# Performance work log

Measured on AMD Instinct MI355X. Metric: run time of the kernel, lower is better.

## Reference

```python
import jax, jax.numpy as jnp
import numpy as np

H, K, D, M = 16, 64, 1024, 4096
S, B = 2048, 4
EPS = 1e-5


def _ln(x, g, b):
    mu = jnp.mean(x, axis=-1, keepdims=True)
    var = jnp.var(x, axis=-1, keepdims=True)
    return (x - mu) / jnp.sqrt(var + EPS) * g + b


def setup_inputs() -> dict:
    key = jax.random.key(0)
    ks = jax.random.split(key, 8)
    std = 0.02
    x = jax.random.normal(ks[0], (S, B, D), jnp.float32)
    mask = jnp.zeros((S, S), jnp.float32)  # additive attention mask, broadcasts over (H*B, S, S)
    wq = jax.random.normal(ks[1], (H * K, D), jnp.float32) * std
    wk = jax.random.normal(ks[2], (H * K, D), jnp.float32) * std
    wv = jax.random.normal(ks[3], (H * K, D), jnp.float32) * std
    wc = jax.random.normal(ks[4], (D, H * K), jnp.float32) * std
    w1_w = jax.random.normal(ks[5], (M, D), jnp.float32) * std
    w1_b = jnp.zeros((M,), jnp.float32)
    w2_w = jax.random.normal(ks[6], (D, M), jnp.float32) * std
    w2_b = jnp.zeros((D,), jnp.float32)
    ln1_g = jnp.ones((D,), jnp.float32)
    ln1_b = jnp.zeros((D,), jnp.float32)
    ln2_g = jnp.ones((D,), jnp.float32)
    ln2_b = jnp.zeros((D,), jnp.float32)
    return dict(x=x, mask=mask, wq=wq, wk=wk, wv=wv, wc=wc, w1_w=w1_w, w1_b=w1_b,
                w2_w=w2_w, w2_b=w2_b, ln1_g=ln1_g, ln1_b=ln1_b, ln2_g=ln2_g, ln2_b=ln2_b)


def reference(x, mask, wq, wk, wv, wc, w1_w, w1_b, w2_w, w2_b, ln1_g, ln1_b, ln2_g, ln2_b):
    s, b, _ = x.shape
    q = (x @ wq.T).reshape(s, b, H, K)
    k = (x @ wk.T).reshape(s, b, H, K)
    v = (x @ wv.T).reshape(s, b, H, K)
    # scores: (B, H, S, S); mask (S, S) broadcasts over batch and heads as in torch
    scores = jnp.einsum('sbhk,tbhk->bhst', q, k) / jnp.sqrt(jnp.float32(K)) + mask
    alpha = jax.nn.softmax(scores, axis=-1)
    av = jnp.einsum('bhst,tbhk->sbhk', alpha, v).reshape(s, b, H * K)
    u = _ln(av @ wc.T + x, ln1_g, ln1_b)
    z = jax.nn.relu(u @ w1_w.T + w1_b) @ w2_w.T + w2_b
    return _ln(z + u, ln2_g, ln2_b)
```

## Files before the change

### kernel.cpp

```cpp
#include <hip/hip_runtime.h>
#include <math.h>

#define H_  16
#define K_  64
#define D_  1024
#define M_  4096
#define S_  2048
#define B_  4
#define N_  8192
#define HK_ 1024

typedef __attribute__((ext_vector_type(8))) short bfrag;
typedef __attribute__((ext_vector_type(4))) float f4;

typedef __attribute__((address_space(1))) const void g_void;
typedef __attribute__((address_space(3))) void s_void;

__device__ __forceinline__ float bf2f(unsigned short u){
  union { unsigned int i; float f; } x; x.i = ((unsigned int)u) << 16; return x.f;
}
__device__ __forceinline__ unsigned short f2bf(float f){
  unsigned int u = __float_as_uint(f);
  return (unsigned short)((u + 0x7fffu + ((u >> 16) & 1u)) >> 16);
}
__device__ __forceinline__ unsigned int pack2(float a, float b){
  return (unsigned int)f2bf(a) | ((unsigned int)f2bf(b) << 16);
}
__device__ __forceinline__ void gload16(const void* g, void* l){
  __builtin_amdgcn_global_load_lds((g_void*)g, (s_void*)l, 16, 0, 0);
}

__global__ __launch_bounds__(256) void castk(const float* __restrict__ in,
                                             unsigned short* __restrict__ out){
  int i = (blockIdx.x * 256 + threadIdx.x) * 4;
  float4 v = *(const float4*)(in + i);
  *(uint2*)(out + i) = make_uint2(pack2(v.x, v.y), pack2(v.z, v.w));
}

__global__ __launch_bounds__(256) void castw4(
    const float* __restrict__ a, const float* __restrict__ b,
    const float* __restrict__ c, const float* __restrict__ d,
    unsigned short* __restrict__ out){
  const int blk = blockIdx.x;
  const int seg = blk >> 10;
  const float* src = (seg == 0) ? a : (seg == 1) ? b : (seg == 2) ? c : d;
  const int rel = ((blk & 1023) * 256 + threadIdx.x) * 4;
  float4 v = *(const float4*)(src + rel);
  *(uint2*)(out + (size_t)seg * 1048576 + rel) = make_uint2(pack2(v.x, v.y), pack2(v.z, v.w));
}

__global__ __launch_bounds__(256) void mscale(const float* __restrict__ in,
                                              float* __restrict__ out){
  int i = (blockIdx.x * 256 + threadIdx.x) * 4;
  float4 v = *(const float4*)(in + i);
  const float c = 1.44269504f;
  v.x *= c; v.y *= c; v.z *= c; v.w *= c;
  *(float4*)(out + i) = v;
}

template<int EPI>
__global__ __launch_bounds__(256) void mgemm(
    const unsigned short* __restrict__ A, const unsigned short* __restrict__ W,
    const float* __restrict__ bias, const void* __restrict__ res,
    unsigned short* __restrict__ C, int Kdim, int Ncols)
{
  __shared__ unsigned short sA[3][4096];
  __shared__ unsigned short sB[3][4096];
  const int tid  = threadIdx.x;
  const int wave = tid >> 6, ln = tid & 63;
  const int lr   = ln & 15, quad = ln >> 4;

  const int nwg = gridDim.x * gridDim.y;
  const int bid = blockIdx.x + gridDim.x * blockIdx.y;
  const int cpx = nwg >> 3;
  const int swz = (bid & 7) * cpx + (bid >> 3);
  const int bx  = swz % gridDim.x, by = swz / gridDim.x;

  const int m0   = by * 128, n0 = bx * 128;
  const int wr   = (wave >> 1) * 64, wc = (wave & 1) * 64;
  const int segr = ln >> 2, segc = (ln & 3) * 8;
  const int sg   = wave * 2;

  const unsigned short* A0 = A + (size_t)(m0 + sg*16      + segr) * Kdim + segc;
  const unsigned short* A1 = A + (size_t)(m0 + sg*16 + 16 + segr) * Kdim + segc;
  const unsigned short* W0 = W + (size_t)(n0 + sg*16      + segr) * Kdim + segc;
  const unsigned short* W1 = W + (size_t)(n0 + sg*16 + 16 + segr) * Kdim + segc;

  const f4 zero = {0.f, 0.f, 0.f, 0.f};
  f4 acc[4][4];
  #pragma unroll
  for (int i=0;i<4;i++)
    #pragma unroll
    for (int j=0;j<4;j++) acc[i][j] = zero;

  auto stage = [&](int buf, int k0){
    gload16(A0 + k0, &sA[buf][sg*512]);
    gload16(A1 + k0, &sA[buf][sg*512 + 512]);
    gload16(W0 + k0, &sB[buf][sg*512]);
    gload16(W1 + k0, &sB[buf][sg*512 + 512]);
  };

  stage(0, 0);
  if (32 < Kdim) stage(1, 32);
  int cur = 0;

  for (int k0 = 0; k0 < Kdim; k0 += 32){
    if (k0 + 32 < Kdim) asm volatile("s_waitcnt vmcnt(4)" ::: "memory");
    else                asm volatile("s_waitcnt vmcnt(0)" ::: "memory");
    __builtin_amdgcn_s_barrier();
    int nxt = cur + 2; if (nxt >= 3) nxt -= 3;
    if (k0 + 64 < Kdim) stage(nxt, k0 + 64);

    bfrag af[4], bf[4];
    #pragma unroll
    for (int i=0;i<4;i++) af[i] = *(const bfrag*)&sA[cur][(wr + i*16 + lr)*32 + quad*8];
    #pragma unroll
    for (int j=0;j<4;j++) bf[j] = *(const bfrag*)&sB[cur][(wc + j*16 + lr)*32 + quad*8];
    #pragma unroll
    for (int i=0;i<4;i++)
      #pragma unroll
      for (int j=0;j<4;j++)
        acc[i][j] = __builtin_amdgcn_mfma_f32_16x16x32_bf16(af[i], bf[j], acc[i][j], 0, 0, 0);
    cur = (cur + 1 == 3) ? 0 : cur + 1;
  }

  #pragma unroll
  for (int i=0;i<4;i++){
    #pragma unroll
    for (int j=0;j<4;j++){
      #pragma unroll
      for (int r=0;r<4;r++){
        const int m = m0 + wr + i*16 + quad*4 + r;
        const int n = n0 + wc + j*16 + lr;
        float t = acc[i][j][r];
        if (EPI == 0){
          const int proj = n >> 10;
          const int s = m >> 2, b = m & 3, h = (n >> 6) & 15, kk = n & 63;
          C[(size_t)proj*8388608 + (((size_t)(b*16 + h)) * S_ + s) * 64 + kk] = f2bf(t);
        } else {
          const size_t off = (size_t)m * Ncols + n;
          if (EPI == 1) t += ((const float*)res)[off];
          if (EPI == 2) t = fmaxf(t + bias[n], 0.f);
          if (EPI == 3) t += bias[n] + bf2f(((const unsigned short*)res)[off]);
          C[off] = f2bf(t);
        }
      }
    }
  }
}

__global__ __launch_bounds__(256) void vtrans(const unsigned short* __restrict__ v,
                                              unsigned short* __restrict__ vT){
  const int tid = threadIdx.x;
  const int wave = tid >> 6, ln = tid & 63;
  const int bh = blockIdx.y;
  const int s  = blockIdx.x * 64 + ln;
  const int d0 = wave * 16;
  unsigned short tmp[16];
  const unsigned short* src = v + ((size_t)bh * S_ + s) * 64 + d0;
  *(uint4*)&tmp[0] = ((const uint4*)src)[0];
  *(uint4*)&tmp[8] = ((const uint4*)src)[1];
  unsigned short* dst = vT + (size_t)bh * 64 * S_ + s;
  #pragma unroll
  for (int e = 0; e < 16; e++)
    dst[(size_t)(d0 + e) * S_] = tmp[e];
}

__global__ __launch_bounds__(256) void fattn(
    const unsigned short* __restrict__ qg, const unsigned short* __restrict__ kg,
    const unsigned short* __restrict__ vT, const float* __restrict__ mb,
    unsigned short* __restrict__ av)
{
  __shared__ unsigned short Ks[2][4096];
  __shared__ unsigned short VTs[2][4096];
  __shared__ unsigned short Ps[4*32*72];
  const int tid  = threadIdx.x;
  const int wave = tid >> 6, ln = tid & 63;
  const int lr   = ln & 15, quad = ln >> 4;
  const int bh   = blockIdx.y;
  const int b    = bh >> 4, h = bh & 15;
  const int s0   = blockIdx.x * 128;
  const size_t base  = (size_t)bh * S_ * 64;
  const size_t tbase = (size_t)bh * 64 * S_;
  const int qw = s0 + wave*32;

  bfrag aq[2][2];
  #pragma unroll
  for (int qb=0;qb<2;qb++)
    #pragma unroll
    for (int hh=0;hh<2;hh++)
      aq[qb][hh] = *(const bfrag*)(qg + base + (size_t)(qw + qb*16 + lr)*64 + hh*32 + quad*8);

  const f4 zero = {0.f, 0.f, 0.f, 0.f};
  f4 acc[2][4];
  #pragma unroll
  for (int qb=0;qb<2;qb++)
    #pragma unroll
    for (int nb=0;nb<4;nb++) acc[qb][nb] = zero;
  float lsum[2][4];
  #pragma unroll
  for (int qb=0;qb<2;qb++)
    #pragma unroll
    for (int r=0;r<4;r++) lsum[qb][r] = 0.f;

  const int strow = wave*16 + (ln >> 3);
  const int scz   = ((ln & 7) ^ (ln >> 3)) * 8;
  const int rxor  = lr & 7;

  unsigned short* const psw = &Ps[wave*2304];

  const float* mrow[2][4];
  #pragma unroll
  for (int qb=0;qb<2;qb++)
    #pragma unroll
    for (int r=0;r<4;r++)
      mrow[qb][r] = mb + (size_t)(qw + qb*16 + quad*4 + r) * S_ + lr;

  auto stage = [&](int bufn, int t0n){
    unsigned short* kd = &Ks[bufn][(wave*16)*64];
    unsigned short* vd = &VTs[bufn][(wave*16)*64];
    gload16(kg + base  + (size_t)(t0n + strow    )*64 + scz, kd);
    gload16(kg + base  + (size_t)(t0n + strow + 8)*64 + scz, kd + 512);
    gload16(vT + tbase + (size_t)(strow    )*S_ + t0n + scz, vd);
    gload16(vT + tbase + (size_t)(strow + 8)*S_ + t0n + scz, vd + 512);
  };

  stage(0, 0);
  int cur = 0;

  for (int t0 = 0; t0 < S_; t0 += 64){
    __syncthreads();

    float mreg[2][4][4];
    #pragma unroll
    for (int qb=0;qb<2;qb++)
      #pragma unroll
      for (int r=0;r<4;r++)
        #pragma unroll
        for (int tb=0;tb<4;tb++)
          mreg[qb][r][tb] = mrow[qb][r][t0 + tb*16];

    if (t0 + 64 < S_) stage(cur ^ 1, t0 + 64);

    const unsigned short* Kc = Ks[cur];
    const unsigned short* Vc = VTs[cur];

    bfrag kf[4][2];
    #pragma unroll
    for (int tb=0;tb<4;tb++)
      #pragma unroll
      for (int hh=0;hh<2;hh++)
        kf[tb][hh] = *(const bfrag*)&Kc[(tb*16 + lr)*64 + (((hh*4 + quad) ^ rxor))*8];

    bfrag vf[4][2];
    #pragma unroll
    for (int nb=0;nb<4;nb++)
      #pragma unroll
      for (int hh=0;hh<2;hh++)
        vf[nb][hh] = *(const bfrag*)&Vc[(nb*16 + lr)*64 + (((hh*4 + quad) ^ rxor))*8];

    #pragma unroll
    for (int qb=0;qb<2;qb++){
      f4 sc[4];
      __builtin_amdgcn_s_setprio(1);
      #pragma unroll
      for (int tb=0;tb<4;tb++){
        f4 t = zero;
        t = __builtin_amdgcn_mfma_f32_16x16x32_bf16(aq[qb][0], kf[tb][0], t, 0, 0, 0);
        t = __builtin_amdgcn_mfma_f32_16x16x32_bf16(aq[qb][1], kf[tb][1], t, 0, 0, 0);
        sc[tb] = t;
      }
      __builtin_amdgcn_s_setprio(0);
      #pragma unroll
      for (int tb=0;tb<4;tb++){
        float p0 = __builtin_amdgcn_exp2f(fmaf(sc[tb][0], 0.18033688f, mreg[qb][0][tb]));
        float p1 = __builtin_amdgcn_exp2f(fmaf(sc[tb][1], 0.18033688f, mreg[qb][1][tb]));
        float p2 = __builtin_amdgcn_exp2f(fmaf(sc[tb][2], 0.18033688f, mreg[qb][2][tb]));
        float p3 = __builtin_amdgcn_exp2f(fmaf(sc[tb][3], 0.18033688f, mreg[qb][3][tb]));
        lsum[qb][0] += p0; lsum[qb][1] += p1;
        lsum[qb][2] += p2; lsum[qb][3] += p3;
        unsigned int pkA, pkB;
        asm("v_cvt_pk_bf16_f32 %0, %1, %2" : "=v"(pkA) : "v"(p0), "v"(p1));
        asm("v_cvt_pk_bf16_f32 %0, %1, %2" : "=v"(pkB) : "v"(p2), "v"(p3));
        unsigned short* pp = &psw[(qb*16 + quad*4)*72 + tb*16 + lr];
        pp[0]   = (unsigned short)pkA;
        pp[72]  = (unsigned short)(pkA >> 16);
        pp[144] = (unsigned short)pkB;
        pp[216] = (unsigned short)(pkB >> 16);
      }
    }

    __builtin_amdgcn_s_setprio(1);
    #pragma unroll
    for (int qb=0;qb<2;qb++){
      bfrag ap0 = *(const bfrag*)&psw[(qb*16 + lr)*72 + quad*8];
      bfrag ap1 = *(const bfrag*)&psw[(qb*16 + lr)*72 + 32 + quad*8];
      #pragma unroll
      for (int nb=0;nb<4;nb++){
        acc[qb][nb] = __builtin_amdgcn_mfma_f32_16x16x32_bf16(ap0, vf[nb][0], acc[qb][nb], 0, 0, 0);
        acc[qb][nb] = __builtin_amdgcn_mfma_f32_16x16x32_bf16(ap1, vf[nb][1], acc[qb][nb], 0, 0, 0);
      }
    }
    __builtin_amdgcn_s_setprio(0);
    cur ^= 1;
  }

  #pragma unroll
  for (int qb=0;qb<2;qb++)
    #pragma unroll
    for (int r=0;r<4;r++){
      float l = lsum[qb][r];
      l += __shfl_xor(l, 1);
      l += __shfl_xor(l, 2);
      l += __shfl_xor(l, 4);
      l += __shfl_xor(l, 8);
      const float inv = 1.f / l;
      const int qrow = qw + qb*16 + quad*4 + r;
      #pragma unroll
      for (int nb=0;nb<4;nb++)
        av[((size_t)qrow * B_ + b) * HK_ + h*64 + nb*16 + lr] = f2bf(acc[qb][nb][r] * inv);
    }
}

template<int OUTF32>
__global__ __launch_bounds__(256) void lnk(
    const unsigned short* __restrict__ pre, const float* __restrict__ g,
    const float* __restrict__ be, void* __restrict__ out)
{
  __shared__ float red[256];
  const int row = blockIdx.x;
  const int tid = threadIdx.x;
  const unsigned short* p = pre + (size_t)row * D_;
  uint2 raw = *(const uint2*)(p + tid*4);
  float x[4] = { bf2f(raw.x & 0xffffu), bf2f(raw.x >> 16),
                 bf2f(raw.y & 0xffffu), bf2f(raw.y >> 16) };
  red[tid] = x[0] + x[1] + x[2] + x[3];
  __syncthreads();
  for (int q = 128; q > 0; q >>= 1){
    if (tid < q) red[tid] += red[tid + q];
    __syncthreads();
  }
  const float mu = red[0] * (1.f / (float)D_);
  __syncthreads();
  float d0 = x[0]-mu, d1 = x[1]-mu, d2 = x[2]-mu, d3 = x[3]-mu;
  red[tid] = d0*d0 + d1*d1 + d2*d2 + d3*d3;
  __syncthreads();
  for (int q = 128; q > 0; q >>= 1){
    if (tid < q) red[tid] += red[tid + q];
    __syncthreads();
  }
  const float rstd = rsqrtf(red[0] * (1.f / (float)D_) + 1e-5f);
  const int c = tid * 4;
  #pragma unroll
  for (int j=0;j<4;j++){
    float y = (x[j] - mu) * rstd * g[c + j] + be[c + j];
    if (OUTF32) ((float*)out)[(size_t)row * D_ + c + j] = y;
    else ((unsigned short*)out)[(size_t)row * D_ + c + j] = f2bf(y);
  }
}

extern "C" void kernel_launch(void* const* d_in, const int* in_sizes, int n_in,
                              void* d_out, int out_size, void* d_ws, size_t ws_size,
                              hipStream_t stream) {
  const float* x    = (const float*)d_in[0];
  const float* mask = (const float*)d_in[1];
  const float* wq   = (const float*)d_in[2];
  const float* wk   = (const float*)d_in[3];
  const float* wv   = (const float*)d_in[4];
  const float* wc   = (const float*)d_in[5];
  const float* w1w  = (const float*)d_in[6];
  const float* w1b  = (const float*)d_in[7];
  const float* w2w  = (const float*)d_in[8];
  const float* w2b  = (const float*)d_in[9];
  const float* g1   = (const float*)d_in[10];
  const float* b1   = (const float*)d_in[11];
  const float* g2   = (const float*)d_in[12];
  const float* b2   = (const float*)d_in[13];

  unsigned short* ws = (unsigned short*)d_ws;
  unsigned short* xb   = ws + 0;
  unsigned short* wqb  = ws + 8388608;
  unsigned short* wkb  = ws + 9437184;
  unsigned short* wvb  = ws + 10485760;
  unsigned short* wcb  = ws + 11534336;
  unsigned short* q    = ws + 12582912;
  unsigned short* k    = ws + 20971520;
  unsigned short* v    = ws + 29360128;
  unsigned short* w1wb = ws + 37748736;
  unsigned short* w2wb = ws + 41943040;
  unsigned short* u    = ws + 46137344;
  unsigned short* z    = ws + 54525952;
  unsigned short* vT   = z;
  unsigned short* avb  = ws + 0;
  unsigned short* t1   = ws + 12582912;
  unsigned short* h1   = ws + 0;
  float*          mb   = (float*)(ws + 46137344);

  castk<<<8192, 256, 0, stream>>>(x,   xb);
  castw4<<<4096, 256, 0, stream>>>(wq, wk, wv, wc, wqb);
  castk<<<4096, 256, 0, stream>>>(w1w, w1wb);
  castk<<<4096, 256, 0, stream>>>(w2w, w2wb);
  mscale<<<4096, 256, 0, stream>>>(mask, mb);

  mgemm<0><<<dim3(24, 64), 256, 0, stream>>>(xb, wqb, nullptr, nullptr, q, D_, 3072);

  vtrans<<<dim3(S_/64, 64), 256, 0, stream>>>(v, vT);
  fattn<<<dim3(S_/128, B_*H_), 256, 0, stream>>>(q, k, vT, mb, avb);

  mgemm<1><<<dim3(8, 64), 256, 0, stream>>>(avb, wcb, nullptr, x, t1, HK_, D_);
  lnk<0><<<dim3(N_), 256, 0, stream>>>(t1, g1, b1, u);

  mgemm<2><<<dim3(32, 64), 256, 0, stream>>>(u, w1wb, w1b, nullptr, h1, D_, M_);

  mgemm<3><<<dim3(8, 64), 256, 0, stream>>>(h1, w2wb, w2b, u, z, M_, D_);
  lnk<1><<<dim3(N_), 256, 0, stream>>>(z, g2, b2, d_out);
}
```

Before: 583.1 us.

## Load V fragments directly from global and compute row sums via MFMA with ones

Removes the shared-memory staging of transposed V: each wave now reads its V fragments straight from global memory (L2/cache-backed) every tile, which halves the LDS footprint and the async copy traffic per stage. The softmax denominator is now computed by an extra MFMA of the bf16 P fragments against a ones vector, replacing per-element fp32 adds and the cross-lane shuffle reduction. The trade-offs are that all four waves redundantly fetch the same V tile from global with exposed latency, and the row sum now uses bf16-rounded probabilities.

```diff
diff --git a/kernel.cpp b/kernel.cpp
--- a/kernel.cpp
+++ b/kernel.cpp
@@ -172,7 +172,6 @@
     unsigned short* __restrict__ av)
 {
   __shared__ unsigned short Ks[2][4096];
-  __shared__ unsigned short VTs[2][4096];
   __shared__ unsigned short Ps[4*32*72];
   const int tid  = threadIdx.x;
   const int wave = tid >> 6, ln = tid & 63;
@@ -192,16 +191,16 @@
       aq[qb][hh] = *(const bfrag*)(qg + base + (size_t)(qw + qb*16 + lr)*64 + hh*32 + quad*8);
 
   const f4 zero = {0.f, 0.f, 0.f, 0.f};
+  const bfrag vones = { (short)0x3F80, (short)0x3F80, (short)0x3F80, (short)0x3F80,
+                        (short)0x3F80, (short)0x3F80, (short)0x3F80, (short)0x3F80 };
   f4 acc[2][4];
-  #pragma unroll
-  for (int qb=0;qb<2;qb++)
+  f4 accL[2];
+  #pragma unroll
+  for (int qb=0;qb<2;qb++){
     #pragma unroll
     for (int nb=0;nb<4;nb++) acc[qb][nb] = zero;
-  float lsum[2][4];
-  #pragma unroll
-  for (int qb=0;qb<2;qb++)
-    #pragma unroll
-    for (int r=0;r<4;r++) lsum[qb][r] = 0.f;
+    accL[qb] = zero;
+  }
 
   const int strow = wave*16 + (ln >> 3);
   const int scz   = ((ln & 7) ^ (ln >> 3)) * 8;
@@ -216,13 +215,12 @@
     for (int r=0;r<4;r++)
       mrow[qb][r] = mb + (size_t)(qw + qb*16 + quad*4 + r) * S_ + lr;
 
+  const unsigned short* vsrc = vT + tbase + (size_t)lr * S_ + quad*8;
+
   auto stage = [&](int bufn, int t0n){
     unsigned short* kd = &Ks[bufn][(wave*16)*64];
-    unsigned short* vd = &VTs[bufn][(wave*16)*64];
-    gload16(kg + base  + (size_t)(t0n + strow    )*64 + scz, kd);
-    gload16(kg + base  + (size_t)(t0n + strow + 8)*64 + scz, kd + 512);
-    gload16(vT + tbase + (size_t)(strow    )*S_ + t0n + scz, vd);
-    gload16(vT + tbase + (size_t)(strow + 8)*S_ + t0n + scz, vd + 512);
+    gload16(kg + base + (size_t)(t0n + strow    )*64 + scz, kd);
+    gload16(kg + base + (size_t)(t0n + strow + 8)*64 + scz, kd + 512);
   };
 
   stage(0, 0);
@@ -230,6 +228,13 @@
 
   for (int t0 = 0; t0 < S_; t0 += 64){
     __syncthreads();
+
+    bfrag vf[4][2];
+    #pragma unroll
+    for (int nb=0;nb<4;nb++)
+      #pragma unroll
+      for (int hh=0;hh<2;hh++)
+        vf[nb][hh] = *(const bfrag*)(vsrc + (size_t)(nb*16) * S_ + t0 + hh*32);
 
     float mreg[2][4][4];
     #pragma unroll
@@ -243,7 +248,6 @@
     if (t0 + 64 < S_) stage(cur ^ 1, t0 + 64);
 
     const unsigned short* Kc = Ks[cur];
-    const unsigned short* Vc = VTs[cur];
 
     bfrag kf[4][2];
     #pragma unroll
@@ -251,13 +255,6 @@
       #pragma unroll
       for (int hh=0;hh<2;hh++)
         kf[tb][hh] = *(const bfrag*)&Kc[(tb*16 + lr)*64 + (((hh*4 + quad) ^ rxor))*8];
-
-    bfrag vf[4][2];
-    #pragma unroll
-    for (int nb=0;nb<4;nb++)
-      #pragma unroll
-      for (int hh=0;hh<2;hh++)
-        vf[nb][hh] = *(const bfrag*)&Vc[(nb*16 + lr)*64 + (((hh*4 + quad) ^ rxor))*8];
 
     #pragma unroll
     for (int qb=0;qb<2;qb++){
@@ -277,8 +274,6 @@
         float p1 = __builtin_amdgcn_exp2f(fmaf(sc[tb][1], 0.18033688f, mreg[qb][1][tb]));
         float p2 = __builtin_amdgcn_exp2f(fmaf(sc[tb][2], 0.18033688f, mreg[qb][2][tb]));
         float p3 = __builtin_amdgcn_exp2f(fmaf(sc[tb][3], 0.18033688f, mreg[qb][3][tb]));
-        lsum[qb][0] += p0; lsum[qb][1] += p1;
-        lsum[qb][2] += p2; lsum[qb][3] += p3;
         unsigned int pkA, pkB;
         asm("v_cvt_pk_bf16_f32 %0, %1, %2" : "=v"(pkA) : "v"(p0), "v"(p1));
         asm("v_cvt_pk_bf16_f32 %0, %1, %2" : "=v"(pkB) : "v"(p2), "v"(p3));
@@ -300,6 +295,8 @@
         acc[qb][nb] = __builtin_amdgcn_mfma_f32_16x16x32_bf16(ap0, vf[nb][0], acc[qb][nb], 0, 0, 0);
         acc[qb][nb] = __builtin_amdgcn_mfma_f32_16x16x32_bf16(ap1, vf[nb][1], acc[qb][nb], 0, 0, 0);
       }
+      accL[qb] = __builtin_amdgcn_mfma_f32_16x16x32_bf16(ap0, vones, accL[qb], 0, 0, 0);
+      accL[qb] = __builtin_amdgcn_mfma_f32_16x16x32_bf16(ap1, vones, accL[qb], 0, 0, 0);
     }
     __builtin_amdgcn_s_setprio(0);
     cur ^= 1;
@@ -309,12 +306,7 @@
   for (int qb=0;qb<2;qb++)
     #pragma unroll
     for (int r=0;r<4;r++){
-      float l = lsum[qb][r];
-      l += __shfl_xor(l, 1);
-      l += __shfl_xor(l, 2);
-      l += __shfl_xor(l, 4);
-      l += __shfl_xor(l, 8);
-      const float inv = 1.f / l;
+      const float inv = 1.f / accL[qb][r];
       const int qrow = qw + qb*16 + quad*4 + r;
       #pragma unroll
       for (int nb=0;nb<4;nb++)
```

Measured after the change: 649.4 us. 1.11x slower.
